# Performance work log

Hardware: AMD Instinct MI355X
Metric: run time of the kernel (lower is better)

The kernel has to match this reference:

```python
import jax, jax.numpy as jnp
import numpy as np

N_RAYS = 65536
NUM_STEPS = 128
UP_STEPS = 128
BOUND = 1.0
MIN_NEAR = 0.05


def _sigma_fn(x, c, log_s, amp):
    # Gaussian blob density: [..., 3] -> [...]
    d2 = jnp.sum((x - c) ** 2, axis=-1)
    return jnp.exp(amp[0]) * jnp.exp(-d2 / (2.0 * jnp.exp(log_s[0]) ** 2))


def _rgb_fn(x, Wc, bc):
    return jax.nn.sigmoid(x @ Wc + bc)


def sample_pdf(bins, weights, n_samples):
    # bins: [N, M+1], weights: [N, M]; deterministic (det=True) inverse-CDF sampling
    w = weights + 1e-5
    pdf = w / jnp.sum(w, axis=-1, keepdims=True)
    cdf = jnp.cumsum(pdf, axis=-1)
    cdf = jnp.concatenate([jnp.zeros_like(cdf[..., :1]), cdf], axis=-1)  # [N, M+1]
    u = jnp.linspace(0.5 / n_samples, 1.0 - 0.5 / n_samples, n_samples, dtype=cdf.dtype)
    u = jnp.broadcast_to(u, cdf.shape[:-1] + (n_samples,))
    inds = jax.vmap(lambda cc, uu: jnp.searchsorted(cc, uu, side='right'))(cdf, u)
    below = jnp.maximum(inds - 1, 0)
    above = jnp.minimum(inds, cdf.shape[-1] - 1)
    cdf_b = jnp.take_along_axis(cdf, below, axis=-1)
    cdf_a = jnp.take_along_axis(cdf, above, axis=-1)
    bins_b = jnp.take_along_axis(bins, below, axis=-1)
    bins_a = jnp.take_along_axis(bins, above, axis=-1)
    denom = cdf_a - cdf_b
    denom = jnp.where(denom < 1e-5, jnp.ones_like(denom), denom)
    t = (u - cdf_b) / denom
    return bins_b + t * (bins_a - bins_b)


def _near_far_from_aabb(rays_o, rays_d):
    safe_d = jnp.where(jnp.abs(rays_d) > 1e-8, rays_d, jnp.sign(rays_d) * 1e-8 + 1e-12)
    inv_d = 1.0 / safe_d
    t1 = (-BOUND - rays_o) * inv_d
    t2 = (BOUND - rays_o) * inv_d
    nears = jnp.max(jnp.minimum(t1, t2), axis=-1)
    fars = jnp.min(jnp.maximum(t1, t2), axis=-1)
    nears = jnp.maximum(nears, MIN_NEAR)
    fars = jnp.maximum(fars, nears + 1e-4)
    return nears[:, None], fars[:, None]


def _composite_weights(z_vals, sigmas, sample_dist):
    deltas = z_vals[..., 1:] - z_vals[..., :-1]
    deltas = jnp.concatenate([deltas, sample_dist * jnp.ones_like(deltas[..., :1])], axis=-1)
    alphas = 1.0 - jnp.exp(-deltas * sigmas)
    shifted = jnp.concatenate([jnp.ones_like(alphas[..., :1]), 1.0 - alphas + 1e-15], axis=-1)
    weights = alphas * jnp.cumprod(shifted, axis=-1)[..., :-1]
    return weights, deltas


def reference(rays_o, rays_d, c, log_s, amp, Wc, bc):
    rays_d = rays_d / jnp.linalg.norm(rays_d, axis=-1, keepdims=True)
    nears, fars = _near_far_from_aabb(rays_o, rays_d)  # [N,1]

    z_vals = nears + (fars - nears) * jnp.linspace(0.0, 1.0, NUM_STEPS, dtype=rays_o.dtype)[None, :]
    sample_dist = (fars - nears) / NUM_STEPS  # [N,1]

    xyzs = rays_o[:, None, :] + rays_d[:, None, :] * z_vals[..., None]
    xyzs = jnp.clip(xyzs, -BOUND, BOUND)
    sigmas = _sigma_fn(xyzs, c, log_s, amp)  # [N, S]

    # coarse weights for importance sampling (no_grad in original)
    weights, deltas = _composite_weights(z_vals, sigmas, sample_dist)
    z_mid = z_vals[..., :-1] + 0.5 * deltas[..., :-1]  # [N, S-1]
    new_z = jax.lax.stop_gradient(sample_pdf(z_mid, jax.lax.stop_gradient(weights[:, 1:-1]), UP_STEPS))

    z_all = jnp.sort(jnp.concatenate([z_vals, new_z], axis=1), axis=1)  # [N, S+U]
    xyzs_all = rays_o[:, None, :] + rays_d[:, None, :] * z_all[..., None]
    xyzs_all = jnp.clip(xyzs_all, -BOUND, BOUND)

    sigmas_all = _sigma_fn(xyzs_all, c, log_s, amp)
    rgbs_all = _rgb_fn(xyzs_all, Wc, bc)

    weights_all, _ = _composite_weights(z_all, sigmas_all, sample_dist)
    weights_sum = jnp.sum(weights_all, axis=-1)  # [N]
    image = jnp.sum(weights_all[..., None] * rgbs_all, axis=1)
    image = image + (1.0 - weights_sum)[..., None]  # white background
    return image


def setup_inputs() -> dict:
    key = jax.random.key(0)
    k1, k2, k3, k4 = jax.random.split(key, 4)
    rays_o = (jax.random.uniform(k1, (N_RAYS, 3), dtype=jnp.float32) - 0.5) * 1.0
    rays_d = jax.random.normal(k2, (N_RAYS, 3), dtype=jnp.float32)
    rays_d = rays_d / jnp.linalg.norm(rays_d, axis=-1, keepdims=True)
    c = 0.2 * jax.random.normal(k3, (3,), dtype=jnp.float32)
    log_s = -1.0 * jnp.ones((1,), dtype=jnp.float32)
    amp = 2.0 * jnp.ones((1,), dtype=jnp.float32)
    Wc = jax.random.normal(k4, (3, 3), dtype=jnp.float32)
    bc = jnp.zeros((3,), dtype=jnp.float32)
    return {"rays_o": rays_o, "rays_d": rays_d, "c": c, "log_s": log_s, "amp": amp, "Wc": Wc, "bc": bc}
```

## Files before the change

### kernel.cpp

```cpp
#include <hip/hip_runtime.h>
#include <math.h>

#define N_RAYS 65536

__device__ __forceinline__ float fast_rcp(float x){ return __builtin_amdgcn_rcpf(x); }
__device__ __forceinline__ float fexp2(float x){
#if __has_builtin(__builtin_amdgcn_exp2f)
    return __builtin_amdgcn_exp2f(x);
#else
    return exp2f(x);
#endif
}

template<int CTRL, int RM = 0xf, int BM = 0xf>
__device__ __forceinline__ float dpp0_f(float src) {
    return __int_as_float(__builtin_amdgcn_update_dpp(
        0, __float_as_int(src), CTRL, RM, BM, true));
}
template<int CTRL, int RM = 0xf, int BM = 0xf>
__device__ __forceinline__ int dppold_i(int old_, int src) {
    return __builtin_amdgcn_update_dpp(old_, src, CTRL, RM, BM, false);
}
template<int OFF>
__device__ __forceinline__ float swz_f(float v) {
    return __int_as_float(__builtin_amdgcn_ds_swizzle(__float_as_int(v), OFF));
}

__device__ __forceinline__ float seg_scan_add(float v) {
    v += dpp0_f<0x111>(v);
    v += dpp0_f<0x112>(v);
    v += dpp0_f<0x114>(v);
    v += dpp0_f<0x118>(v);
    return v;
}
__device__ __forceinline__ float seg_scan_max(float v) {
    v = fmaxf(v, dpp0_f<0x111>(v));
    v = fmaxf(v, dpp0_f<0x112>(v));
    v = fmaxf(v, dpp0_f<0x114>(v));
    v = fmaxf(v, dpp0_f<0x118>(v));
    return v;
}

__global__ __launch_bounds__(256) void nerf_wave9_kernel(
    const float* __restrict__ rays_o, const float* __restrict__ rays_d,
    const float* __restrict__ cptr, const float* __restrict__ log_s,
    const float* __restrict__ amp, const float* __restrict__ Wc,
    const float* __restrict__ bcp, float* __restrict__ out)
{
    const int li = (int)(threadIdx.x & 15u);
    const int pr = (int)(threadIdx.x >> 4);
    const int ray = (int)(blockIdx.x << 4) + pr;

    __shared__ __align__(16) float su[16*256];
    float* __restrict__ ub   = su + (pr << 8);
    float* __restrict__ cdf  = ub;
    float* __restrict__ bins = ub + 128;
    float* __restrict__ zall = ub;

    *reinterpret_cast<float4*>(&bins[8*li])   = make_float4(0.f,0.f,0.f,0.f);
    *reinterpret_cast<float4*>(&bins[8*li+4]) = make_float4(0.f,0.f,0.f,0.f);

    float ox = rays_o[ray*3+0], oy = rays_o[ray*3+1], oz = rays_o[ray*3+2];
    float dx = rays_d[ray*3+0], dy = rays_d[ray*3+1], dz = rays_d[ray*3+2];
    float inv_n = rsqrtf(dx*dx + dy*dy + dz*dz);
    dx *= inv_n; dy *= inv_n; dz *= inv_n;

    const float L2E = 1.4426950408889634f;
    float ccx = cptr[0], ccy = cptr[1], ccz = cptr[2];
    float inv2s2 = 0.5f * fexp2(-2.0f * L2E * log_s[0]);
    float ampv = amp[0];
    float w00 = Wc[0], w01 = Wc[1], w02 = Wc[2];
    float w10 = Wc[3], w11 = Wc[4], w12 = Wc[5];
    float w20 = Wc[6], w21 = Wc[7], w22 = Wc[8];
    float b0 = bcp[0], b1 = bcp[1], b2 = bcp[2];

    float ex = ox - ccx, ey = oy - ccy, ez = oz - ccz;
    float gam = ex*ex + ey*ey + ez*ez;
    float ddte = dx*ex + dy*ey + dz*ez;
    float Q2 = -inv2s2 * L2E;
    float Q1 = -2.f * ddte * inv2s2 * L2E;
    float S0 = (ampv - gam * inv2s2) * L2E + 0.52876637294489777f;

    float dot0 = dx*w00 + dy*w10 + dz*w20;
    float dot1 = dx*w01 + dy*w11 + dz*w21;
    float dot2 = dx*w02 + dy*w12 + dz*w22;
    float U0 = (ox*w00 + oy*w10 + oz*w20 + b0) * L2E;
    float U1 = (ox*w01 + oy*w11 + oz*w21 + b1) * L2E;
    float U2 = (ox*w02 + oy*w12 + oz*w22 + b2) * L2E;
    float V0 = dot0 * L2E, V1 = dot1 * L2E, V2 = dot2 * L2E;

    auto safe_inv = [](float d) {
        float sg = (d > 0.f) ? 1.f : ((d < 0.f) ? -1.f : 0.f);
        float sd = (fabsf(d) > 1e-8f) ? d : (sg * 1e-8f + 1e-12f);
        return fast_rcp(sd);
    };
    float ixv = safe_inv(dx), iyv = safe_inv(dy), izv = safe_inv(dz);
    float t1x = (-1.f - ox) * ixv, t2x = (1.f - ox) * ixv;
    float t1y = (-1.f - oy) * iyv, t2y = (1.f - oy) * iyv;
    float t1z = (-1.f - oz) * izv, t2z = (1.f - oz) * izv;
    float nearz = fmaxf(fmaxf(fminf(t1x,t2x), fminf(t1y,t2y)), fminf(t1z,t2z));
    float farz  = fminf(fminf(fmaxf(t1x,t2x), fmaxf(t1y,t2y)), fmaxf(t1z,t2z));
    nearz = fmaxf(nearz, 0.05f);
    farz  = fmaxf(farz, nearz + 1e-4f);

    float span = farz - nearz;
    float step = span * (1.0f/127.0f);
    float inv_step = fast_rcp(step);
    float sample_dist = span * (1.0f/128.0f);

    const float lif = (float)li;
    const float i0f = 8.f*lif;
    float psq[8];
    {
        float zz = fmaf(step, i0f, nearz);
        float pp = 0.f;
        #pragma unroll
        for (int q = 0; q < 8; q++) {
            float s2 = fexp2(fmaf(zz, fmaf(zz,Q2,Q1), S0));
            float dl = (q == 7 && li == 15) ? sample_dist : step;
            pp = fmaf(dl, s2, pp);
            psq[q] = pp;
            zz += step;
        }
    }
    float tauI = seg_scan_add(psq[7]);
    float tauE = tauI - psq[7];

    float Tm[8];
    #pragma unroll
    for (int q = 0; q < 8; q++) Tm[q] = fexp2(-(tauE + psq[q]));
    float T1   = swz_f<0x010>(Tm[0]);
    float T127 = swz_f<0x1F0>(Tm[6]);
    float wsum = T1 - T127 + 126e-5f;
    float invw = fast_rcp(wsum);
    float k5 = 1e-5f * invw;

    float cv[8];
    #pragma unroll
    for (int q = 0; q < 8; q++)
        cv[q] = fmaf(i0f + (float)q, k5, (T1 - Tm[q]) * invw);
    *reinterpret_cast<float4*>(&cdf[8*li])   = make_float4(cv[0],cv[1],cv[2],cv[3]);
    *reinterpret_cast<float4*>(&cdf[8*li+4]) = make_float4(cv[4],cv[5],cv[6],cv[7]);

    {
        int rr[8];
        #pragma unroll
        for (int q = 0; q < 8; q++)
            rr[q] = (int)ceilf(fmaf(128.f, cv[q], -0.5f));
        if (li == 15) rr[7] = 999;
        int rn = dppold_i<0x101>(999, rr[0]);
        float mv = i0f + 1.f;
        #pragma unroll
        for (int q = 0; q < 7; q++)
            if (rr[q] != rr[q+1] && rr[q] <= 127) bins[rr[q]] = mv + (float)q;
        if (rr[7] != rn && rr[7] <= 127) bins[rr[7]] = mv + 7.f;
    }

    float fz[8]; int isl[8];
    {
        float4 bb0 = *reinterpret_cast<const float4*>(&bins[8*li]);
        float4 bb1 = *reinterpret_cast<const float4*>(&bins[8*li+4]);
        float m0 = bb0.x;
        float m1 = fmaxf(m0, bb0.y);
        float m2 = fmaxf(m1, bb0.z);
        float m3 = fmaxf(m2, bb0.w);
        float m4 = fmaxf(m3, bb1.x);
        float m5 = fmaxf(m4, bb1.y);
        float m6 = fmaxf(m5, bb1.z);
        float m7 = fmaxf(m6, bb1.w);
        float Mi = seg_scan_max(m7);
        float Me = dpp0_f<0x111>(Mi);
        float A[8] = { fmaxf(Me,m0), fmaxf(Me,m1), fmaxf(Me,m2), fmaxf(Me,m3),
                       fmaxf(Me,m4), fmaxf(Me,m5), fmaxf(Me,m6), fmaxf(Me,m7) };
        int blo[8];
        float cb[8], car[8];
        #pragma unroll
        for (int q = 0; q < 8; q++) blo[q] = (int)A[q] - 1;
        #pragma unroll
        for (int q = 0; q < 8; q++) { cb[q] = cdf[blo[q]]; car[q] = cdf[blo[q]+1]; }
        float uL = fmaf(lif, 0.0625f, 0.00390625f);
        #pragma unroll
        for (int q = 0; q < 8; q++) {
            float u = fmaf((float)q, 0.0078125f, uL);
            bool valid = (blo[q] <= 125);
            float d_ba = valid ? step : 0.f;
            float dn   = valid ? (car[q] - cb[q]) : 0.f;
            float dn2  = (dn < 1e-5f) ? 1.f : dn;
            float tt = (u - cb[q]) * fast_rcp(dn2);
            float zb = fmaf(step, A[q] - 0.5f, nearz);
            fz[q] = fmaf(tt, d_ba, zb);
            float cntf = floorf((fz[q] - nearz) * inv_step) + 1.f;
            isl[q] = 8*li + q + (int)cntf;
        }
    }

    {
        float4 m4v = make_float4(-1.f,-1.f,-1.f,-1.f);
        *reinterpret_cast<float4*>(&zall[16*li])    = m4v;
        *reinterpret_cast<float4*>(&zall[16*li+4])  = m4v;
        *reinterpret_cast<float4*>(&zall[16*li+8])  = m4v;
        *reinterpret_cast<float4*>(&zall[16*li+12]) = m4v;
    }
    #pragma unroll
    for (int q = 0; q < 8; q++) zall[isl[q]] = fz[q];

    float zt[16];
    {
        float4 a0 = *reinterpret_cast<const float4*>(&zall[16*li]);
        float4 a1 = *reinterpret_cast<const float4*>(&zall[16*li+4]);
        float4 a2 = *reinterpret_cast<const float4*>(&zall[16*li+8]);
        float4 a3 = *reinterpret_cast<const float4*>(&zall[16*li+12]);
        zt[0]=a0.x; zt[1]=a0.y; zt[2]=a0.z; zt[3]=a0.w;
        zt[4]=a1.x; zt[5]=a1.y; zt[6]=a1.z; zt[7]=a1.w;
        zt[8]=a2.x; zt[9]=a2.y; zt[10]=a2.z; zt[11]=a2.w;
        zt[12]=a3.x; zt[13]=a3.y; zt[14]=a3.z; zt[15]=a3.w;
    }
    float fsum = 0.f;
    #pragma unroll
    for (int q = 0; q < 16; q++) fsum += (zt[q] >= 0.f) ? 1.f : 0.f;
    float incl3 = seg_scan_add(fsum);
    float runf = incl3 - fsum;

    float pbase = 16.f*lif;
    #pragma unroll
    for (int q = 0; q < 16; q++) {
        float fgq = (zt[q] >= 0.f) ? 1.f : 0.f;
        float cif = pbase + (float)q - runf;
        float zc = fmaf(step, cif, nearz);
        zt[q] = (fgq > 0.f) ? zt[q] : zc;
        runf += fgq;
    }
    float ztE = dpp0_f<0x101>(zt[0]);

    float pps[16];
    {
        float pp = 0.f;
        #pragma unroll
        for (int q = 0; q < 16; q++) {
            float s2 = fexp2(fmaf(zt[q], fmaf(zt[q], Q2, Q1), S0));
            float delta = (q < 15) ? (zt[q+1] - zt[q])
                                   : ((li < 15) ? (ztE - zt[15]) : sample_dist);
            pp = fmaf(delta, s2, pp);
            pps[q] = pp;
        }
    }
    float tauI3 = seg_scan_add(pps[15]);
    float tauE3 = tauI3 - pps[15];

    float T16 = fexp2(-tauI3);
    float Tprev = dpp0_f<0x111>(T16);
    if (li == 0) Tprev = 1.f;
    float Tw0 = Tprev;

    float rA = 0.f, gA = 0.f, bA = 0.f;
    #pragma unroll
    for (int h = 0; h < 4; h++) {
        const int qb = 4*h;
        float ze = zt[qb];
        float Ta = fexp2(-(tauE3 + pps[qb]));
        float Tb = fexp2(-(tauE3 + pps[qb+1]));
        float Tc = fexp2(-(tauE3 + pps[qb+2]));
        float Td = (h == 3) ? T16 : fexp2(-(tauE3 + pps[qb+3]));
        float wq0 = Tprev - Ta, wq1 = Ta - Tb, wq2 = Tb - Tc, wq3 = Tc - Td;
        Tprev = Td;
        float s0 = fast_rcp(1.f + fexp2(-fmaf(V0, ze, U0)));
        float s1 = fast_rcp(1.f + fexp2(-fmaf(V1, ze, U1)));
        float s2 = fast_rcp(1.f + fexp2(-fmaf(V2, ze, U2)));
        float g0 = fmaf(-s0, s0, s0);
        float g1 = fmaf(-s1, s1, s1);
        float g2 = fmaf(-s2, s2, s2);
        float dz1 = zt[qb+1] - ze, dz2 = zt[qb+2] - ze, dz3 = zt[qb+3] - ze;
        float wsh = ((wq0 + wq1) + wq2) + wq3;
        float wdz = fmaf(wq1, dz1, fmaf(wq2, dz2, wq3 * dz3));
        rA = fmaf(s0, wsh, fmaf(g0 * dot0, wdz, rA));
        gA = fmaf(s1, wsh, fmaf(g1 * dot1, wdz, gA));
        bA = fmaf(s2, wsh, fmaf(g2 * dot2, wdz, bA));
    }
    float wA = Tw0 - T16;

    rA += dpp0_f<0xB1>(rA);  gA += dpp0_f<0xB1>(gA);
    bA += dpp0_f<0xB1>(bA);  wA += dpp0_f<0xB1>(wA);
    rA += dpp0_f<0x4E>(rA);  gA += dpp0_f<0x4E>(gA);
    bA += dpp0_f<0x4E>(bA);  wA += dpp0_f<0x4E>(wA);
    int sel = li & 3;
    float v = rA;
    v = (sel == 1) ? gA : v;
    v = (sel == 2) ? bA : v;
    v = (sel == 3) ? wA : v;
    v += dpp0_f<0x124>(v);
    v += dpp0_f<0x128>(v);
    float wtot = swz_f<0x070>(v);
    if (li < 3) out[ray*3 + li] = v + (1.f - wtot);
}

extern "C" void kernel_launch(void* const* d_in, const int* in_sizes, int n_in,
                              void* d_out, int out_size, void* d_ws, size_t ws_size,
                              hipStream_t stream) {
    const float* rays_o = (const float*)d_in[0];
    const float* rays_d = (const float*)d_in[1];
    const float* c      = (const float*)d_in[2];
    const float* log_s  = (const float*)d_in[3];
    const float* amp    = (const float*)d_in[4];
    const float* Wc     = (const float*)d_in[5];
    const float* bc     = (const float*)d_in[6];
    float* out = (float*)d_out;

    dim3 block(256);
    dim3 grid(N_RAYS / 16);
    hipLaunchKernelGGL(nerf_wave9_kernel, grid, block, 0, stream,
                       rays_o, rays_d, c, log_s, amp, Wc, bc, out);
}
```

Before: 31.59 us.

## Pack quantized CDF values with bin index into max-scan keys

Each bin boundary now writes packed integer keys to shared memory: the CDF value quantized to 23 bits, shifted left, with the bin index in the low bits, plus a second key holding the next CDF value. An integer max-scan then yields the lower index and both CDF endpoints directly, so the 16 dependent LDS gathers of cdf[below] and cdf[below+1] are no longer needed. The background term now comes from the final transmittance broadcast from the last lane rather than a reduced weight sum, which drops one reduction channel. Quantizing the CDF to 2^-23 steps slightly changes sample positions, and left-shifting by 7 can overflow if a CDF value reaches 1.0.

```diff
diff --git a/kernel.cpp b/kernel.cpp
--- a/kernel.cpp
+++ b/kernel.cpp
@@ -18,6 +18,10 @@
         0, __float_as_int(src), CTRL, RM, BM, true));
 }
 template<int CTRL, int RM = 0xf, int BM = 0xf>
+__device__ __forceinline__ int dpp0_i(int src) {
+    return __builtin_amdgcn_update_dpp(0, src, CTRL, RM, BM, true);
+}
+template<int CTRL, int RM = 0xf, int BM = 0xf>
 __device__ __forceinline__ int dppold_i(int old_, int src) {
     return __builtin_amdgcn_update_dpp(old_, src, CTRL, RM, BM, false);
 }
@@ -33,15 +37,15 @@
     v += dpp0_f<0x118>(v);
     return v;
 }
-__device__ __forceinline__ float seg_scan_max(float v) {
-    v = fmaxf(v, dpp0_f<0x111>(v));
-    v = fmaxf(v, dpp0_f<0x112>(v));
-    v = fmaxf(v, dpp0_f<0x114>(v));
-    v = fmaxf(v, dpp0_f<0x118>(v));
+__device__ __forceinline__ int seg_scan_max_i(int v) {
+    v = max(v, dpp0_i<0x111>(v));
+    v = max(v, dpp0_i<0x112>(v));
+    v = max(v, dpp0_i<0x114>(v));
+    v = max(v, dpp0_i<0x118>(v));
     return v;
 }
 
-__global__ __launch_bounds__(256) void nerf_wave9_kernel(
+__global__ __launch_bounds__(256) void nerf_waveA_kernel(
     const float* __restrict__ rays_o, const float* __restrict__ rays_d,
     const float* __restrict__ cptr, const float* __restrict__ log_s,
     const float* __restrict__ amp, const float* __restrict__ Wc,
@@ -53,12 +57,17 @@
 
     __shared__ __align__(16) float su[16*256];
     float* __restrict__ ub   = su + (pr << 8);
-    float* __restrict__ cdf  = ub;
-    float* __restrict__ bins = ub + 128;
+    int*   __restrict__ keyL = (int*)ub;
+    int*   __restrict__ keyH = (int*)(ub + 128);
     float* __restrict__ zall = ub;
 
-    *reinterpret_cast<float4*>(&bins[8*li])   = make_float4(0.f,0.f,0.f,0.f);
-    *reinterpret_cast<float4*>(&bins[8*li+4]) = make_float4(0.f,0.f,0.f,0.f);
+    {
+        int4 z4 = make_int4(0,0,0,0);
+        *reinterpret_cast<int4*>(&keyL[16*li])   = z4;
+        *reinterpret_cast<int4*>(&keyL[16*li+4]) = z4;
+        *reinterpret_cast<int4*>(&keyL[16*li+8]) = z4;
+        *reinterpret_cast<int4*>(&keyL[16*li+12])= z4;
+    }
 
     float ox = rays_o[ray*3+0], oy = rays_o[ray*3+1], oz = rays_o[ray*3+2];
     float dx = rays_d[ray*3+0], dy = rays_d[ray*3+1], dz = rays_d[ray*3+2];
@@ -139,8 +148,12 @@
     #pragma unroll
     for (int q = 0; q < 8; q++)
         cv[q] = fmaf(i0f + (float)q, k5, (T1 - Tm[q]) * invw);
-    *reinterpret_cast<float4*>(&cdf[8*li])   = make_float4(cv[0],cv[1],cv[2],cv[3]);
-    *reinterpret_cast<float4*>(&cdf[8*li+4]) = make_float4(cv[4],cv[5],cv[6],cv[7]);
+
+    int qk[8];
+    #pragma unroll
+    for (int q = 0; q < 8; q++) qk[q] = (int)(cv[q] * 8388608.f);
+    float cv0n = dpp0_f<0x101>(cv[0]);
+    int qkN = (int)(cv0n * 8388608.f);
 
     {
         int rr[8];
@@ -149,45 +162,55 @@
             rr[q] = (int)ceilf(fmaf(128.f, cv[q], -0.5f));
         if (li == 15) rr[7] = 999;
         int rn = dppold_i<0x101>(999, rr[0]);
-        float mv = i0f + 1.f;
-        #pragma unroll
-        for (int q = 0; q < 7; q++)
-            if (rr[q] != rr[q+1] && rr[q] <= 127) bins[rr[q]] = mv + (float)q;
-        if (rr[7] != rn && rr[7] <= 127) bins[rr[7]] = mv + 7.f;
+        int m0i = 8*li;
+        #pragma unroll
+        for (int q = 0; q < 7; q++) {
+            if (rr[q] != rr[q+1] && rr[q] <= 127) {
+                keyL[rr[q]] = (qk[q] << 7) | (m0i + q);
+                keyH[rr[q]] = qk[q+1] << 7;
+            }
+        }
+        if (rr[7] != rn && rr[7] <= 127) {
+            keyL[rr[7]] = (qk[7] << 7) | (m0i + 7);
+            keyH[rr[7]] = qkN << 7;
+        }
     }
 
     float fz[8]; int isl[8];
     {
-        float4 bb0 = *reinterpret_cast<const float4*>(&bins[8*li]);
-        float4 bb1 = *reinterpret_cast<const float4*>(&bins[8*li+4]);
-        float m0 = bb0.x;
-        float m1 = fmaxf(m0, bb0.y);
-        float m2 = fmaxf(m1, bb0.z);
-        float m3 = fmaxf(m2, bb0.w);
-        float m4 = fmaxf(m3, bb1.x);
-        float m5 = fmaxf(m4, bb1.y);
-        float m6 = fmaxf(m5, bb1.z);
-        float m7 = fmaxf(m6, bb1.w);
-        float Mi = seg_scan_max(m7);
-        float Me = dpp0_f<0x111>(Mi);
-        float A[8] = { fmaxf(Me,m0), fmaxf(Me,m1), fmaxf(Me,m2), fmaxf(Me,m3),
-                       fmaxf(Me,m4), fmaxf(Me,m5), fmaxf(Me,m6), fmaxf(Me,m7) };
-        int blo[8];
-        float cb[8], car[8];
-        #pragma unroll
-        for (int q = 0; q < 8; q++) blo[q] = (int)A[q] - 1;
-        #pragma unroll
-        for (int q = 0; q < 8; q++) { cb[q] = cdf[blo[q]]; car[q] = cdf[blo[q]+1]; }
+        int4 kb0 = *reinterpret_cast<const int4*>(&keyL[8*li]);
+        int4 kb1 = *reinterpret_cast<const int4*>(&keyL[8*li+4]);
+        int4 kh0 = *reinterpret_cast<const int4*>(&keyH[8*li]);
+        int4 kh1 = *reinterpret_cast<const int4*>(&keyH[8*li+4]);
+        int nL[8], nH[8];
+        nL[0] = kb0.x;              nH[0] = kh0.x;
+        nL[1] = max(nL[0], kb0.y);  nH[1] = max(nH[0], kh0.y);
+        nL[2] = max(nL[1], kb0.z);  nH[2] = max(nH[1], kh0.z);
+        nL[3] = max(nL[2], kb0.w);  nH[3] = max(nH[2], kh0.w);
+        nL[4] = max(nL[3], kb1.x);  nH[4] = max(nH[3], kh1.x);
+        nL[5] = max(nL[4], kb1.y);  nH[5] = max(nH[4], kh1.y);
+        nL[6] = max(nL[5], kb1.z);  nH[6] = max(nH[5], kh1.z);
+        nL[7] = max(nL[6], kb1.w);  nH[7] = max(nH[6], kh1.w);
+        int MiL = seg_scan_max_i(nL[7]);
+        int MiH = seg_scan_max_i(nH[7]);
+        int MeL = dpp0_i<0x111>(MiL);
+        int MeH = dpp0_i<0x111>(MiH);
+        const float Q23 = 1.1920928955078125e-7f;
         float uL = fmaf(lif, 0.0625f, 0.00390625f);
         #pragma unroll
         for (int q = 0; q < 8; q++) {
+            int AL = max(MeL, nL[q]);
+            int AH = max(MeH, nH[q]);
+            int below = AL & 127;
+            float cb  = (float)(AL >> 7) * Q23;
+            float car = (float)(AH >> 7) * Q23;
             float u = fmaf((float)q, 0.0078125f, uL);
-            bool valid = (blo[q] <= 125);
+            bool valid = (below <= 125);
             float d_ba = valid ? step : 0.f;
-            float dn   = valid ? (car[q] - cb[q]) : 0.f;
+            float dn   = valid ? (car - cb) : 0.f;
             float dn2  = (dn < 1e-5f) ? 1.f : dn;
-            float tt = (u - cb[q]) * fast_rcp(dn2);
-            float zb = fmaf(step, A[q] - 0.5f, nearz);
+            float tt = (u - cb) * fast_rcp(dn2);
+            float zb = fmaf(step, (float)below + 0.5f, nearz);
             fz[q] = fmaf(tt, d_ba, zb);
             float cntf = floorf((fz[q] - nearz) * inv_step) + 1.f;
             isl[q] = 8*li + q + (int)cntf;
@@ -250,7 +273,6 @@
     float T16 = fexp2(-tauI3);
     float Tprev = dpp0_f<0x111>(T16);
     if (li == 0) Tprev = 1.f;
-    float Tw0 = Tprev;
 
     float rA = 0.f, gA = 0.f, bA = 0.f;
     #pragma unroll
@@ -276,21 +298,17 @@
         gA = fmaf(s1, wsh, fmaf(g1 * dot1, wdz, gA));
         bA = fmaf(s2, wsh, fmaf(g2 * dot2, wdz, bA));
     }
-    float wA = Tw0 - T16;
-
-    rA += dpp0_f<0xB1>(rA);  gA += dpp0_f<0xB1>(gA);
-    bA += dpp0_f<0xB1>(bA);  wA += dpp0_f<0xB1>(wA);
-    rA += dpp0_f<0x4E>(rA);  gA += dpp0_f<0x4E>(gA);
-    bA += dpp0_f<0x4E>(bA);  wA += dpp0_f<0x4E>(wA);
+
+    rA += dpp0_f<0xB1>(rA);  gA += dpp0_f<0xB1>(gA);  bA += dpp0_f<0xB1>(bA);
+    rA += dpp0_f<0x4E>(rA);  gA += dpp0_f<0x4E>(gA);  bA += dpp0_f<0x4E>(bA);
     int sel = li & 3;
     float v = rA;
     v = (sel == 1) ? gA : v;
     v = (sel == 2) ? bA : v;
-    v = (sel == 3) ? wA : v;
     v += dpp0_f<0x124>(v);
     v += dpp0_f<0x128>(v);
-    float wtot = swz_f<0x070>(v);
-    if (li < 3) out[ray*3 + li] = v + (1.f - wtot);
+    float bgT = swz_f<0x1F0>(T16);
+    if (li < 3) out[ray*3 + li] = v + bgT;
 }
 
 extern "C" void kernel_launch(void* const* d_in, const int* in_sizes, int n_in,
@@ -307,6 +325,6 @@
 
     dim3 block(256);
     dim3 grid(N_RAYS / 16);
-    hipLaunchKernelGGL(nerf_wave9_kernel, grid, block, 0, stream,
+    hipLaunchKernelGGL(nerf_waveA_kernel, grid, block, 0, stream,
                        rays_o, rays_d, c, log_s, amp, Wc, bc, out);
 }
```

New measurement: 33.01 us. +4.5%, slower.
